# Optimization experiments

Hardware: AMD Instinct MI355X
Metric: run time of the kernel (lower is better)

The kernel has to match this reference:

```python
import math
import jax, jax.numpy as jnp
import numpy as np

TWO_PI = 2.0 * math.pi


def make_coords(H, W):
    """Replicates ConvNet.generate_coordinates -> offsets of shape (9, 2, H, W).
    Pair k gives (dy, dx) for kernel tap k (row-major 3x3); center tap (k=4) is zero."""
    gy, gx = jnp.meshgrid(jnp.arange(H, dtype=jnp.float32),
                          jnp.arange(W, dtype=jnp.float32), indexing='ij')
    cy = H / 2.0 - 0.5
    cx = W / 2.0 - 0.5
    # torch: delta_x along height, delta_y along width; theta = atan2(dy, dx) mod 2pi
    theta = jnp.arctan2(gx - cx, gy - cy) % TWO_PI
    theta = jnp.round(theta * 10000.0) / 10000.0
    # per-tap (angle multiple m of pi/4, additive (ay, ax)); tap 4 (center) stays zero
    taps = [(0, 1.0, 1.0), (1, 1.0, 0.0), (2, 1.0, -1.0), (3, 0.0, 1.0), None,
            (4, 0.0, -1.0), (5, -1.0, 1.0), (6, -1.0, 0.0), (7, -1.0, -1.0)]
    offs = []
    zero = jnp.zeros_like(theta)
    for t in taps:
        if t is None:
            offs.append(jnp.stack([zero, zero]))
        else:
            m, ay, ax = t
            ang = theta + (math.pi / 4.0) * m
            offs.append(jnp.stack([jnp.cos(ang) + ay, jnp.sin(ang) + ax]))
    return jnp.stack(offs)  # (9, 2, H, W)


def deform_conv(x, off, w):
    """torchvision.ops.deform_conv2d, 3x3, stride 1, pad 1, dilation 1, no bias.
    x: (B,C,H,W), off: (9,2,H,W), w: (O,C,3,3) -> (B,O,H,W)."""
    B, C, H, W = x.shape
    ky = jnp.repeat(jnp.arange(3, dtype=jnp.float32), 3)  # (9,)
    kx = jnp.tile(jnp.arange(3, dtype=jnp.float32), 3)
    # sampling positions (H, W, 9)
    py = (jnp.arange(H, dtype=jnp.float32)[:, None, None] - 1.0
          + ky[None, None, :] + jnp.transpose(off[:, 0], (1, 2, 0)))
    px = (jnp.arange(W, dtype=jnp.float32)[None, :, None] - 1.0
          + kx[None, None, :] + jnp.transpose(off[:, 1], (1, 2, 0)))
    y0 = jnp.floor(py)
    x0 = jnp.floor(px)
    wy = py - y0  # bilinear weights
    wx = px - x0

    def gather(yf, xf):
        valid = (yf >= 0) & (yf <= H - 1) & (xf >= 0) & (xf <= W - 1)
        yi = jnp.clip(yf, 0, H - 1).astype(jnp.int32)
        xi = jnp.clip(xf, 0, W - 1).astype(jnp.int32)
        return x[:, :, yi, xi] * valid.astype(x.dtype)  # (B,C,H,W,9)

    sampled = ((1 - wy) * (1 - wx) * gather(y0, x0)
               + (1 - wy) * wx * gather(y0, x0 + 1)
               + wy * (1 - wx) * gather(y0 + 1, x0)
               + wy * wx * gather(y0 + 1, x0 + 1))
    return jnp.einsum('bchwk,ock->bohw', sampled, w.reshape(w.shape[0], C, 9))


def maxpool2(x):
    B, C, H, W = x.shape
    return x.reshape(B, C, H // 2, 2, W // 2, 2).max(axis=(3, 5))


def setup_inputs() -> dict:
    key = jax.random.key(0)
    ks = jax.random.split(key, 20)

    def kaiming(k, shape):
        fan_in = int(np.prod(shape[1:]))
        return jax.random.normal(k, shape, jnp.float32) * np.float32(np.sqrt(2.0 / fan_in))

    inp = {'x': jax.random.normal(ks[0], (8, 3, 128, 128), jnp.float32)}
    conv_shapes = [('w11', (64, 3, 3, 3)), ('w12', (64, 64, 3, 3)),
                   ('w21', (128, 64, 3, 3)), ('w22', (128, 128, 3, 3)),
                   ('w31', (256, 128, 3, 3)), ('w32', (256, 256, 3, 3)), ('w33', (256, 256, 3, 3)),
                   ('w41', (512, 256, 3, 3)), ('w42', (512, 512, 3, 3)), ('w43', (512, 512, 3, 3)),
                   ('w51', (512, 512, 3, 3)), ('w52', (512, 512, 3, 3)), ('w53', (512, 512, 3, 3))]
    for i, (n, s) in enumerate(conv_shapes):
        inp[n] = kaiming(ks[i + 1], s)
    inp['fc1_w'] = kaiming(ks[14], (4096, 512))
    inp['fc1_b'] = jnp.zeros((4096,), jnp.float32)
    inp['fc2_w'] = kaiming(ks[15], (4096, 4096))
    inp['fc2_b'] = jnp.zeros((4096,), jnp.float32)
    inp['fc3_w'] = kaiming(ks[16], (30, 4096))
    inp['fc3_b'] = jnp.zeros((30,), jnp.float32)
    return inp


def reference(x, w11, w12, w21, w22, w31, w32, w33, w41, w42, w43,
              w51, w52, w53, fc1_w, fc1_b, fc2_w, fc2_b, fc3_w, fc3_b):
    c128 = make_coords(128, 128)
    c64 = make_coords(64, 64)
    c32 = make_coords(32, 32)
    c16 = make_coords(16, 16)
    c8 = make_coords(8, 8)
    r = jax.nn.relu
    x = r(deform_conv(x, c128, w11))
    x = r(deform_conv(x, c128, w12))
    x = maxpool2(x)
    x = r(deform_conv(x, c64, w21))
    x = r(deform_conv(x, c64, w22))
    x = maxpool2(x)
    x = r(deform_conv(x, c32, w31))
    x = r(deform_conv(x, c32, w32))
    x = r(deform_conv(x, c32, w33))
    x = maxpool2(x)
    x = r(deform_conv(x, c16, w41))
    x = r(deform_conv(x, c16, w42))
    x = r(deform_conv(x, c16, w43))
    x = maxpool2(x)
    x = r(deform_conv(x, c8, w51))
    x = r(deform_conv(x, c8, w52))
    x = r(deform_conv(x, c8, w53))
    x = maxpool2(x)          # -> (B, 512, 4, 4)
    x = x.mean(axis=(2, 3))  # AvgPool2d((4,4)) on 4x4 -> (B, 512)
    x = r(x @ fc1_w.T + fc1_b)
    x = r(x @ fc2_w.T + fc2_b)
    return x @ fc3_w.T + fc3_b  # (B, 30)
```

## Files before the change

### kernel.cpp

```cpp
#include <hip/hip_runtime.h>
#include <math.h>

#define TWO_PI_F 6.283185307179586f
#define PI_4_F   0.7853981633974483f

typedef __attribute__((ext_vector_type(8))) short short8;
typedef __attribute__((ext_vector_type(4))) float f32x4;
typedef __attribute__((ext_vector_type(2))) float f32x2;
typedef __attribute__((ext_vector_type(4))) unsigned short ushort4v;
typedef __attribute__((ext_vector_type(4))) unsigned int uint4v;
typedef __attribute__((ext_vector_type(2))) unsigned int uint2v;

struct Tap { int i00, i01, i10, i11; float w00, w01, w10, w11; };

static __device__ __forceinline__ unsigned short f2bf(float f) {
    unsigned u = __builtin_bit_cast(unsigned, f);
    u = (u + 0x7fffu + ((u >> 16) & 1u)) >> 16;
    return (unsigned short)u;
}
static __device__ __forceinline__ float bf2f(unsigned short u) {
    return __builtin_bit_cast(float, (unsigned)u << 16);
}
static __device__ __forceinline__ f32x2 up2(unsigned u) {
    f32x2 r;
    r.x = __builtin_bit_cast(float, u << 16);
    r.y = __builtin_bit_cast(float, u & 0xffff0000u);
    return r;
}
static __device__ __forceinline__ unsigned cvt_pk_bf16(float lo, float hi) {
    unsigned r;
    asm("v_cvt_pk_bf16_f32 %0, %1, %2" : "=v"(r) : "v"(lo), "v"(hi));
    return r;
}

__global__ void build_table_kernel(Tap* __restrict__ tab, int* __restrict__ tabA, int S) {
    int idx = blockIdx.x * blockDim.x + threadIdx.x;
    int total = S * S * 9;
    if (idx >= total) return;
    int k = idx % 9;
    int p = idx / 9;
    int y = p / S;
    int x = p - y * S;
    int HW = S * S;

    float c = 0.5f * (float)S - 0.5f;
    float theta = atan2f((float)x - c, (float)y - c);
    theta = fmodf(theta, TWO_PI_F);
    if (theta < 0.0f) theta += TWO_PI_F;
    theta = rintf(theta * 10000.0f) / 10000.0f;

    float offy = 0.0f, offx = 0.0f;
    if (k != 4) {
        int m = (k < 4) ? k : (k - 1);
        const float ayt[8] = { 1.f, 1.f,  1.f, 0.f,  0.f, -1.f, -1.f, -1.f };
        const float axt[8] = { 1.f, 0.f, -1.f, 1.f, -1.f,  1.f,  0.f, -1.f };
        float ang = theta + PI_4_F * (float)m;
        offy = cosf(ang) + ayt[m];
        offx = sinf(ang) + axt[m];
    }
    int ky = k / 3, kx = k - ky * 3;
    float py = (float)y - 1.0f + (float)ky + offy;
    float px = (float)x - 1.0f + (float)kx + offx;
    float fy0 = floorf(py), fx0 = floorf(px);
    float wy = py - fy0, wx = px - fx0;
    float fmaxc = (float)(S - 1);

    Tap t;
    {
        float yy = fy0, xx = fx0;
        bool v = (yy >= 0.f) && (yy <= fmaxc) && (xx >= 0.f) && (xx <= fmaxc);
        int yi = (int)fminf(fmaxf(yy, 0.f), fmaxc);
        int xi = (int)fminf(fmaxf(xx, 0.f), fmaxc);
        t.i00 = yi * S + xi;
        t.w00 = v ? (1.f - wy) * (1.f - wx) : 0.f;
    }
    {
        float yy = fy0, xx = fx0 + 1.0f;
        bool v = (yy >= 0.f) && (yy <= fmaxc) && (xx >= 0.f) && (xx <= fmaxc);
        int yi = (int)fminf(fmaxf(yy, 0.f), fmaxc);
        int xi = (int)fminf(fmaxf(xx, 0.f), fmaxc);
        t.i01 = yi * S + xi;
        t.w01 = v ? (1.f - wy) * wx : 0.f;
    }
    {
        float yy = fy0 + 1.0f, xx = fx0;
        bool v = (yy >= 0.f) && (yy <= fmaxc) && (xx >= 0.f) && (xx <= fmaxc);
        int yi = (int)fminf(fmaxf(yy, 0.f), fmaxc);
        int xi = (int)fminf(fmaxf(xx, 0.f), fmaxc);
        t.i10 = yi * S + xi;
        t.w10 = v ? wy * (1.f - wx) : 0.f;
    }
    {
        float yy = fy0 + 1.0f, xx = fx0 + 1.0f;
        bool v = (yy >= 0.f) && (yy <= fmaxc) && (xx >= 0.f) && (xx <= fmaxc);
        int yi = (int)fminf(fmaxf(yy, 0.f), fmaxc);
        int xi = (int)fminf(fmaxf(xx, 0.f), fmaxc);
        t.i11 = yi * S + xi;
        t.w11 = v ? wy * wx : 0.f;
    }
    tab[idx] = t;

    int rec = (k * HW + p) * 8;
    tabA[rec + 0] = t.i00;
    tabA[rec + 1] = t.i01;
    tabA[rec + 2] = t.i10;
    tabA[rec + 3] = t.i11;
    tabA[rec + 4] = __builtin_bit_cast(int, t.w00);
    tabA[rec + 5] = __builtin_bit_cast(int, t.w01);
    tabA[rec + 6] = __builtin_bit_cast(int, t.w10);
    tabA[rec + 7] = __builtin_bit_cast(int, t.w11);
}

__global__ void pack_w_kernel(const float* __restrict__ w, unsigned short* __restrict__ wP,
                              int O, int C, int total) {
    int idx = blockIdx.x * blockDim.x + threadIdx.x;
    if (idx >= total) return;
    int ksub = idx & 31;
    int kbo  = idx >> 5;
    int o  = kbo % O;
    int kb = kbo / O;
    int K = kb * 32 + ksub;
    int kt = K / C;
    int c  = K - kt * C;
    wP[idx] = f2bf(w[((size_t)o * C + c) * 9 + kt]);
}

__global__ __launch_bounds__(256) void dconv_f32_kernel(
    const float* __restrict__ x, const float* __restrict__ w,
    const Tap* __restrict__ tab, unsigned short* __restrict__ out,
    int C, int O, int HW)
{
    __shared__ float4 sTabRaw[64 * 9 * 2];
    __shared__ float  sS[9][64];
    __shared__ float  sW[9][64];

    const int tid = threadIdx.x;
    const int b  = blockIdx.z;
    const int o0 = blockIdx.y * 64;
    const int p0 = blockIdx.x * 64;
    const int C9 = C * 9;

    const float4* gt = (const float4*)(tab + (size_t)p0 * 9);
    for (int i = tid; i < 64 * 9 * 2; i += 256) sTabRaw[i] = gt[i];
    const Tap* sTab = (const Tap*)sTabRaw;
    __syncthreads();

    float acc[4][4];
#pragma unroll
    for (int i = 0; i < 4; ++i)
#pragma unroll
        for (int j = 0; j < 4; ++j) acc[i][j] = 0.f;

    const int to = tid >> 4;
    const int tn = tid & 15;
    const float* xb = x + (size_t)b * C * HW;

    for (int c = 0; c < C; ++c) {
        const float* xp = xb + (size_t)c * HW;
        for (int i = tid; i < 9 * 64; i += 256) {
            int k = i >> 6;
            int p = i & 63;
            Tap t = sTab[p * 9 + k];
            sS[k][p] = t.w00 * xp[t.i00] + t.w01 * xp[t.i01]
                     + t.w10 * xp[t.i10] + t.w11 * xp[t.i11];
        }
        for (int i = tid; i < 9 * 64; i += 256) {
            int k = i >> 6;
            int o = i & 63;
            sW[k][o] = w[(size_t)(o0 + o) * C9 + c * 9 + k];
        }
        __syncthreads();
#pragma unroll
        for (int k = 0; k < 9; ++k) {
            float4 wv = *(const float4*)&sW[k][to * 4];
            float4 sv = *(const float4*)&sS[k][tn * 4];
            acc[0][0] += wv.x * sv.x; acc[0][1] += wv.x * sv.y; acc[0][2] += wv.x * sv.z; acc[0][3] += wv.x * sv.w;
            acc[1][0] += wv.y * sv.x; acc[1][1] += wv.y * sv.y; acc[1][2] += wv.y * sv.z; acc[1][3] += wv.y * sv.w;
            acc[2][0] += wv.z * sv.x; acc[2][1] += wv.z * sv.y; acc[2][2] += wv.z * sv.z; acc[2][3] += wv.z * sv.w;
            acc[3][0] += wv.w * sv.x; acc[3][1] += wv.w * sv.y; acc[3][2] += wv.w * sv.z; acc[3][3] += wv.w * sv.w;
        }
        __syncthreads();
    }

    const int ob   = (o0 + to * 4) >> 3;
    const int osub = (to & 1) << 2;
#pragma unroll
    for (int j = 0; j < 4; ++j) {
        int p = p0 + tn * 4 + j;
        ushort4v v;
        v.x = f2bf(fmaxf(acc[0][j], 0.f));
        v.y = f2bf(fmaxf(acc[1][j], 0.f));
        v.z = f2bf(fmaxf(acc[2][j], 0.f));
        v.w = f2bf(fmaxf(acc[3][j], 0.f));
        *(ushort4v*)(out + (((size_t)b * (O >> 3) + ob) * HW + p) * 8 + osub) = v;
    }
}

#define SPITCH 296

template<int BM>
__global__ __launch_bounds__(256, 4) void dconv_mfma(
    const unsigned short* __restrict__ x, const unsigned short* __restrict__ wP,
    const int* __restrict__ tabA, unsigned short* __restrict__ out,
    float* __restrict__ part,
    int C, int O, int HW, int Cchunk, int nChunks)
{
    __shared__ unsigned short sS[64 * SPITCH];

    const int tid  = threadIdx.x;
    const int lane = tid & 63;
    const int wv   = tid >> 6;
    const int bz = blockIdx.z;
    const int b     = bz & 7;
    const int chunk = bz >> 3;

    int bx = blockIdx.x;
    const int gx = gridDim.x;
    if ((gx & 7) == 0) { int g8 = gx >> 3; bx = (bx & 7) * g8 + (bx >> 3); }

    const int o0 = blockIdx.y * BM;
    const int p0 = bx * 64;
    const int c0 = chunk * Cchunk;
    const int nGroups = Cchunk >> 5;

    const int o0w = (BM == 128) ? wv * 32 : (wv >> 1) * 32;
    const int p0w = (BM == 128) ? 0       : (wv & 1) * 32;
    constexpr int MF = 2;
    constexpr int NF = (BM == 128) ? 4 : 2;

    f32x4 acc[MF][NF] = {};

    const unsigned short* xb = x + (size_t)b * C * HW;
    const int quad = lane >> 4;
    const int l16  = lane & 15;
    const int* tq = tabA + (((size_t)(p0 + lane)) << 3);
    unsigned short* srow = &sS[lane * SPITCH + (wv << 3)];

    for (int g = 0; g < nGroups; ++g) {
        const int cg = c0 + g * 32;
        const unsigned short* xcb = xb + ((((size_t)(cg >> 3) + wv) * HW) << 3);

#pragma unroll 3
        for (int kt = 0; kt < 9; ++kt) {
            const int* tp = tq + kt * (HW << 3);
            int4 ii = *(const int4*)tp;
            int4 iw = *(const int4*)(tp + 4);
            float w00 = __builtin_bit_cast(float, iw.x);
            float w01 = __builtin_bit_cast(float, iw.y);
            float w10 = __builtin_bit_cast(float, iw.z);
            float w11 = __builtin_bit_cast(float, iw.w);
            uint4v g00 = *(const uint4v*)(xcb + ((size_t)ii.x << 3));
            uint4v g01 = *(const uint4v*)(xcb + ((size_t)ii.y << 3));
            uint4v g10 = *(const uint4v*)(xcb + ((size_t)ii.z << 3));
            uint4v g11 = *(const uint4v*)(xcb + ((size_t)ii.w << 3));
            uint4v pk;
#pragma unroll
            for (int wd = 0; wd < 4; ++wd) {
                f32x2 s = up2(g00[wd]) * w00 + up2(g01[wd]) * w01
                        + up2(g10[wd]) * w10 + up2(g11[wd]) * w11;
                pk[wd] = cvt_pk_bf16(s.x, s.y);
            }
            *(uint4v*)(srow + kt * 32) = pk;
        }
        __syncthreads();

#pragma unroll 3
        for (int kt = 0; kt < 9; ++kt) {
            const int kb = (kt * C + cg) >> 5;
            short8 afr[MF], bfr[NF];
#pragma unroll
            for (int mf = 0; mf < MF; ++mf) {
                int orow = o0 + o0w + mf * 16 + l16;
                afr[mf] = *(const short8*)(wP + (((size_t)kb * O + orow) << 5) + (quad << 3));
            }
#pragma unroll
            for (int nf = 0; nf < NF; ++nf) {
                int prow = p0w + nf * 16 + l16;
                bfr[nf] = *(const short8*)(&sS[prow * SPITCH + kt * 32 + (quad << 3)]);
            }
#pragma unroll
            for (int mf = 0; mf < MF; ++mf)
#pragma unroll
                for (int nf = 0; nf < NF; ++nf)
                    acc[mf][nf] = __builtin_amdgcn_mfma_f32_16x16x32_bf16(afr[mf], bfr[nf], acc[mf][nf], 0, 0, 0);
        }
        __syncthreads();
    }

    const int O8 = O >> 3;
    if (nChunks == 1) {
#pragma unroll
        for (int mf = 0; mf < MF; ++mf)
#pragma unroll
            for (int nf = 0; nf < NF; ++nf) {
                int o = o0 + o0w + mf * 16 + (quad << 2);
                int p = p0 + p0w + nf * 16 + l16;
                size_t base = (((size_t)b * O8 + (o >> 3)) * HW + p) * 8 + (o & 7);
                uint2v pk2;
                pk2.x = cvt_pk_bf16(fmaxf(acc[mf][nf][0], 0.f), fmaxf(acc[mf][nf][1], 0.f));
                pk2.y = cvt_pk_bf16(fmaxf(acc[mf][nf][2], 0.f), fmaxf(acc[mf][nf][3], 0.f));
                *(uint2v*)(out + base) = pk2;
            }
    } else {
        float* pb = part + (size_t)chunk * 8 * O * HW;
#pragma unroll
        for (int mf = 0; mf < MF; ++mf)
#pragma unroll
            for (int nf = 0; nf < NF; ++nf) {
                int o = o0 + o0w + mf * 16 + (quad << 2);
                int p = p0 + p0w + nf * 16 + l16;
                size_t base = (((size_t)b * O8 + (o >> 3)) * HW + p) * 8 + (o & 7);
                *(f32x4*)(pb + base) = acc[mf][nf];
            }
    }
}

__global__ void reduce_relu_kernel(const float* __restrict__ part,
                                   unsigned short* __restrict__ out,
                                   int per4, int nChunks)
{
    int idx = blockIdx.x * blockDim.x + threadIdx.x;
    if (idx >= per4) return;
    const float4* p4 = (const float4*)part;
    float4 s = p4[idx];
    for (int ch = 1; ch < nChunks; ++ch) {
        float4 v = p4[(size_t)ch * per4 + idx];
        s.x += v.x; s.y += v.y; s.z += v.z; s.w += v.w;
    }
    ushort4v r;
    r.x = f2bf(fmaxf(s.x, 0.f)); r.y = f2bf(fmaxf(s.y, 0.f));
    r.z = f2bf(fmaxf(s.z, 0.f)); r.w = f2bf(fmaxf(s.w, 0.f));
    ((ushort4v*)out)[idx] = r;
}

__global__ void reduce_relu_pool_kernel(const float* __restrict__ part,
                                        unsigned short* __restrict__ out,
                                        int S, int per, int nChunks, int total)
{
    int idx = blockIdx.x * blockDim.x + threadIdx.x;
    if (idx >= total) return;
    int Sl = 31 - __clz(S);
    int W2 = S >> 1;
    int c8 = idx & 7;
    int t  = idx >> 3;
    int x2 = t & (W2 - 1); t >>= (Sl - 1);
    int y2 = t & (W2 - 1); t >>= (Sl - 1);
    size_t base = (((size_t)t * S + 2 * y2) * S + 2 * x2) * 8 + c8;
    size_t dX = 8;
    size_t dY = (size_t)S * 8;
    float s0 = 0.f, s1 = 0.f, s2 = 0.f, s3 = 0.f;
    for (int ch = 0; ch < nChunks; ++ch) {
        const float* p = part + (size_t)ch * per + base;
        s0 += p[0]; s1 += p[dX]; s2 += p[dY]; s3 += p[dY + dX];
    }
    out[idx] = f2bf(fmaxf(fmaxf(fmaxf(s0, s1), fmaxf(s2, s3)), 0.f));
}

__global__ void maxpool_kernel(const unsigned short* __restrict__ in,
                               unsigned short* __restrict__ out,
                               int S, int total)
{
    int idx = blockIdx.x * blockDim.x + threadIdx.x;
    if (idx >= total) return;
    int Sl = 31 - __clz(S);
    int W2 = S >> 1;
    int c8 = idx & 7;
    int t  = idx >> 3;
    int x2 = t & (W2 - 1); t >>= (Sl - 1);
    int y2 = t & (W2 - 1); t >>= (Sl - 1);
    size_t base = (((size_t)t * S + 2 * y2) * S + 2 * x2) * 8 + c8;
    size_t dY = (size_t)S * 8;
    const unsigned short* p = in + base;
    float m = fmaxf(fmaxf(bf2f(p[0]), bf2f(p[8])), fmaxf(bf2f(p[dY]), bf2f(p[dY + 8])));
    out[idx] = f2bf(m);
}

__global__ void avgpool_kernel(const unsigned short* __restrict__ in,
                               float* __restrict__ out, int total)
{
    int idx = blockIdx.x * blockDim.x + threadIdx.x;
    if (idx >= total) return;
    int b = idx >> 9;
    int c = idx & 511;
    int cb = c >> 3, c8 = c & 7;
    const unsigned short* p = in + (((size_t)(b * 64 + cb) * 16) << 3) + c8;
    float s = 0.f;
#pragma unroll
    for (int i = 0; i < 16; ++i) s += bf2f(p[i * 8]);
    out[idx] = s * (1.0f / 16.0f);
}

__global__ __launch_bounds__(256) void fc_kernel(
    const float* __restrict__ x, const float* __restrict__ w,
    const float* __restrict__ bias, float* __restrict__ out,
    int K, int O, int relu)
{
    int o = blockIdx.x;
    float acc[8] = {0.f,0.f,0.f,0.f,0.f,0.f,0.f,0.f};
    const float* wr = w + (size_t)o * K;
    for (int k = threadIdx.x; k < K; k += 256) {
        float wv = wr[k];
#pragma unroll
        for (int b = 0; b < 8; ++b) acc[b] += wv * x[(size_t)b * K + k];
    }
    __shared__ float red[8][256];
#pragma unroll
    for (int b = 0; b < 8; ++b) red[b][threadIdx.x] = acc[b];
    __syncthreads();
    for (int s = 128; s > 0; s >>= 1) {
        if (threadIdx.x < s) {
#pragma unroll
            for (int b = 0; b < 8; ++b) red[b][threadIdx.x] += red[b][threadIdx.x + s];
        }
        __syncthreads();
    }
    if (threadIdx.x < 8) {
        float v = red[threadIdx.x][0] + bias[o];
        if (relu) v = fmaxf(v, 0.f);
        out[(size_t)threadIdx.x * O + o] = v;
    }
}

extern "C" void kernel_launch(void* const* d_in, const int* in_sizes, int n_in,
                              void* d_out, int out_size, void* d_ws, size_t ws_size,
                              hipStream_t stream) {
    const float* x    = (const float*)d_in[0];
    const float* wf[13];
    for (int i = 0; i < 13; ++i) wf[i] = (const float*)d_in[1 + i];
    const float* fc1w = (const float*)d_in[14];
    const float* fc1b = (const float*)d_in[15];
    const float* fc2w = (const float*)d_in[16];
    const float* fc2b = (const float*)d_in[17];
    const float* fc3w = (const float*)d_in[18];
    const float* fc3b = (const float*)d_in[19];
    float* out = (float*)d_out;

    char* ws = (char*)d_ws;
    auto alloc = [&](size_t bytes) -> char* {
        char* p = ws;
        ws += (bytes + 255) & ~(size_t)255;
        return p;
    };

    const int sizes[5] = {128, 64, 32, 16, 8};
    Tap* tabs[5];
    int* tabAs[5];
    for (int i = 0; i < 5; ++i) {
        int HW = sizes[i] * sizes[i];
        tabs[i]  = (Tap*)alloc((size_t)HW * 9 * sizeof(Tap));
        tabAs[i] = (int*)alloc((size_t)HW * 9 * 8 * sizeof(int));
    }
    unsigned short* actA = (unsigned short*)alloc((size_t)8 * 64 * 128 * 128 * 2);
    unsigned short* actB = (unsigned short*)alloc((size_t)8 * 64 * 128 * 128 * 2);
    float* partial = (float*)alloc((size_t)2 * 8 * 128 * 4096 * sizeof(float));
    const int Cs[13] = {3, 64, 64, 128, 128, 256, 256, 256, 512, 512, 512, 512, 512};
    const int Os[13] = {64, 64, 128, 128, 256, 256, 256, 512, 512, 512, 512, 512, 512};
    unsigned short* wPk[13];
    wPk[0] = nullptr;
    for (int i = 1; i < 13; ++i)
        wPk[i] = (unsigned short*)alloc((size_t)Os[i] * Cs[i] * 9 * sizeof(unsigned short));
    float* pooled = (float*)alloc((size_t)8 * 512 * sizeof(float));
    float* fcb1 = (float*)alloc((size_t)8 * 4096 * sizeof(float));
    float* fcb2 = (float*)alloc((size_t)8 * 4096 * sizeof(float));

    for (int i = 0; i < 5; ++i) {
        int total = sizes[i] * sizes[i] * 9;
        build_table_kernel<<<(total + 255) / 256, 256, 0, stream>>>(tabs[i], tabAs[i], sizes[i]);
    }
    for (int i = 1; i < 13; ++i) {
        int total = Os[i] * Cs[i] * 9;
        pack_w_kernel<<<(total + 255) / 256, 256, 0, stream>>>(wf[i], wPk[i], Os[i], Cs[i], total);
    }

    auto convM = [&](const unsigned short* in, const unsigned short* wp, int* tabA,
                     unsigned short* o, int C, int O, int S, int nCh, int BM, bool leavePartial) {
        int HW = S * S;
        int Cchunk = C / nCh;
        if (BM == 64) {
            dim3 grid(HW / 64, O / 64, 8 * nCh);
            dconv_mfma<64><<<grid, 256, 0, stream>>>(in, wp, tabA, o, partial, C, O, HW, Cchunk, nCh);
        } else {
            dim3 grid(HW / 64, O / 128, 8 * nCh);
            dconv_mfma<128><<<grid, 256, 0, stream>>>(in, wp, tabA, o, partial, C, O, HW, Cchunk, nCh);
        }
        if (nCh > 1 && !leavePartial) {
            int per4 = 8 * O * HW / 4;
            reduce_relu_kernel<<<(per4 + 255) / 256, 256, 0, stream>>>(partial, o, per4, nCh);
        }
    };
    auto fusedPool = [&](unsigned short* o, int C, int H, int nCh) {
        int per = 8 * C * H * H;
        int total = per / 4;
        reduce_relu_pool_kernel<<<(total + 255) / 256, 256, 0, stream>>>(partial, o, H, per, nCh, total);
    };

    {
        dim3 grid(128 * 128 / 64, 1, 8);
        dconv_f32_kernel<<<grid, 256, 0, stream>>>(x, wf[0], tabs[0], actA, 3, 64, 128 * 128);
    }
    convM(actA, wPk[1],  tabAs[0], actB, 64,  64,  128, 1, 64, false);
    {
        int total = 8 * 64 * 64 * 64;
        maxpool_kernel<<<(total + 255) / 256, 256, 0, stream>>>(actB, actA, 128, total);
    }
    convM(actA, wPk[2],  tabAs[1], actB, 64,  128, 64, 2, 128, false);
    convM(actB, wPk[3],  tabAs[1], nullptr, 128, 128, 64, 2, 128, true);
    fusedPool(actA, 128, 64, 2);
    convM(actA, wPk[4],  tabAs[2], actB, 128, 256, 32, 4, 128, false);
    convM(actB, wPk[5],  tabAs[2], actA, 256, 256, 32, 4, 128, false);
    convM(actA, wPk[6],  tabAs[2], nullptr, 256, 256, 32, 4, 128, true);
    fusedPool(actB, 256, 32, 4);
    convM(actB, wPk[7],  tabAs[3], actA, 256, 512, 16, 8, 128, false);
    convM(actA, wPk[8],  tabAs[3], actB, 512, 512, 16, 8, 128, false);
    convM(actB, wPk[9],  tabAs[3], nullptr, 512, 512, 16, 8, 128, true);
    fusedPool(actA, 512, 16, 8);
    convM(actA, wPk[10], tabAs[4], actB, 512, 512, 8, 16, 64, false);
    convM(actB, wPk[11], tabAs[4], actA, 512, 512, 8, 16, 64, false);
    convM(actA, wPk[12], tabAs[4], nullptr, 512, 512, 8, 16, 64, true);
    fusedPool(actB, 512, 8, 16);

    avgpool_kernel<<<(4096 + 255) / 256, 256, 0, stream>>>(actB, pooled, 8 * 512);

    fc_kernel<<<4096, 256, 0, stream>>>(pooled, fc1w, fc1b, fcb1, 512,  4096, 1);
    fc_kernel<<<4096, 256, 0, stream>>>(fcb1,   fc2w, fc2b, fcb2, 4096, 4096, 1);
    fc_kernel<<<30,   256, 0, stream>>>(fcb2,   fc3w, fc3b, out,  4096, 30,   0);
}
```

Before: 700.0 us.

## Batch table/weight-pack launches and hoist tap indices, skip center-tap interpolation

Merges the five per-scale table-building launches into one 2D-grid launch, and the twelve weight-packing launches into one launch that uses a cumulative-offset lookup. In the MFMA deformable conv kernel, the per-tap gather indices are loaded once into registers before the channel-group loop instead of being reloaded for every group. The center tap (offset zero) becomes a direct copy with no bilinear blend. The aim is to cut launch overhead and redundant table loads, at the cost of higher register pressure from holding nine int4 values.

```diff
diff --git a/kernel.cpp b/kernel.cpp
--- a/kernel.cpp
+++ b/kernel.cpp
@@ -33,10 +33,18 @@
     return r;
 }
 
-__global__ void build_table_kernel(Tap* __restrict__ tab, int* __restrict__ tabA, int S) {
+struct TabPtrs { Tap* tab[5]; int* tabA[5]; };
+
+__global__ void build_table_all(TabPtrs tp) {
+    const int Ss[5] = {128, 64, 32, 16, 8};
+    int si = blockIdx.y;
+    int S = Ss[si];
     int idx = blockIdx.x * blockDim.x + threadIdx.x;
     int total = S * S * 9;
     if (idx >= total) return;
+    Tap* __restrict__ tab  = tp.tab[si];
+    int* __restrict__ tabA = tp.tabA[si];
+
     int k = idx % 9;
     int p = idx / 9;
     int y = p / S;
@@ -111,18 +119,33 @@
     tabA[rec + 7] = __builtin_bit_cast(int, t.w11);
 }
 
-__global__ void pack_w_kernel(const float* __restrict__ w, unsigned short* __restrict__ wP,
-                              int O, int C, int total) {
+struct PackArgs {
+    const float* w[12];
+    unsigned short* wP[12];
+    int O[12];
+    int C[12];
+    int tot[12];
+};
+
+__global__ void pack_w_all(PackArgs pa, int grand) {
     int idx = blockIdx.x * blockDim.x + threadIdx.x;
-    if (idx >= total) return;
-    int ksub = idx & 31;
-    int kbo  = idx >> 5;
+    if (idx >= grand) return;
+    int li = 0, base = 0;
+#pragma unroll
+    for (int i = 0; i < 11; ++i) {
+        if (idx >= pa.tot[i]) { li = i + 1; base = pa.tot[i]; }
+    }
+    int rel = idx - base;
+    int O = pa.O[li];
+    int C = pa.C[li];
+    int ksub = rel & 31;
+    int kbo  = rel >> 5;
     int o  = kbo % O;
     int kb = kbo / O;
     int K = kb * 32 + ksub;
     int kt = K / C;
     int c  = K - kt * C;
-    wP[idx] = f2bf(w[((size_t)o * C + c) * 9 + kt]);
+    pa.wP[li][rel] = f2bf(pa.w[li][((size_t)o * C + c) * 9 + kt]);
 }
 
 __global__ __launch_bounds__(256) void dconv_f32_kernel(
@@ -235,6 +258,12 @@
     const int l16  = lane & 15;
     const int* tq = tabA + (((size_t)(p0 + lane)) << 3);
     unsigned short* srow = &sS[lane * SPITCH + (wv << 3)];
+    const int HW8 = HW << 3;
+
+    int4 iiA[9];
+#pragma unroll
+    for (int kt = 0; kt < 9; ++kt)
+        iiA[kt] = *(const int4*)(tq + kt * HW8);
 
     for (int g = 0; g < nGroups; ++g) {
         const int cg = c0 + g * 32;
@@ -242,25 +271,28 @@
 
 #pragma unroll 3
         for (int kt = 0; kt < 9; ++kt) {
-            const int* tp = tq + kt * (HW << 3);
-            int4 ii = *(const int4*)tp;
-            int4 iw = *(const int4*)(tp + 4);
-            float w00 = __builtin_bit_cast(float, iw.x);
-            float w01 = __builtin_bit_cast(float, iw.y);
-            float w10 = __builtin_bit_cast(float, iw.z);
-            float w11 = __builtin_bit_cast(float, iw.w);
-            uint4v g00 = *(const uint4v*)(xcb + ((size_t)ii.x << 3));
-            uint4v g01 = *(const uint4v*)(xcb + ((size_t)ii.y << 3));
-            uint4v g10 = *(const uint4v*)(xcb + ((size_t)ii.z << 3));
-            uint4v g11 = *(const uint4v*)(xcb + ((size_t)ii.w << 3));
-            uint4v pk;
-#pragma unroll
-            for (int wd = 0; wd < 4; ++wd) {
-                f32x2 s = up2(g00[wd]) * w00 + up2(g01[wd]) * w01
-                        + up2(g10[wd]) * w10 + up2(g11[wd]) * w11;
-                pk[wd] = cvt_pk_bf16(s.x, s.y);
+            int4 ii = iiA[kt];
+            if (kt == 4) {
+                *(uint4v*)(srow + kt * 32) = *(const uint4v*)(xcb + ((size_t)ii.x << 3));
+            } else {
+                int4 iw = *(const int4*)(tq + kt * HW8 + 4);
+                float w00 = __builtin_bit_cast(float, iw.x);
+                float w01 = __builtin_bit_cast(float, iw.y);
+                float w10 = __builtin_bit_cast(float, iw.z);
+                float w11 = __builtin_bit_cast(float, iw.w);
+                uint4v g00 = *(const uint4v*)(xcb + ((size_t)ii.x << 3));
+                uint4v g01 = *(const uint4v*)(xcb + ((size_t)ii.y << 3));
+                uint4v g10 = *(const uint4v*)(xcb + ((size_t)ii.z << 3));
+                uint4v g11 = *(const uint4v*)(xcb + ((size_t)ii.w << 3));
+                uint4v pk;
+#pragma unroll
+                for (int wd = 0; wd < 4; ++wd) {
+                    f32x2 s = up2(g00[wd]) * w00 + up2(g01[wd]) * w01
+                            + up2(g10[wd]) * w10 + up2(g11[wd]) * w11;
+                    pk[wd] = cvt_pk_bf16(s.x, s.y);
+                }
+                *(uint4v*)(srow + kt * 32) = pk;
             }
-            *(uint4v*)(srow + kt * 32) = pk;
         }
         __syncthreads();
 
@@ -463,13 +495,24 @@
     float* fcb1 = (float*)alloc((size_t)8 * 4096 * sizeof(float));
     float* fcb2 = (float*)alloc((size_t)8 * 4096 * sizeof(float));
 
-    for (int i = 0; i < 5; ++i) {
-        int total = sizes[i] * sizes[i] * 9;
-        build_table_kernel<<<(total + 255) / 256, 256, 0, stream>>>(tabs[i], tabAs[i], sizes[i]);
-    }
-    for (int i = 1; i < 13; ++i) {
-        int total = Os[i] * Cs[i] * 9;
-        pack_w_kernel<<<(total + 255) / 256, 256, 0, stream>>>(wf[i], wPk[i], Os[i], Cs[i], total);
+    {
+        TabPtrs tp;
+        for (int i = 0; i < 5; ++i) { tp.tab[i] = tabs[i]; tp.tabA[i] = tabAs[i]; }
+        dim3 grid((128 * 128 * 9 + 255) / 256, 5);
+        build_table_all<<<grid, 256, 0, stream>>>(tp);
+    }
+    {
+        PackArgs pa;
+        int cum = 0;
+        for (int i = 0; i < 12; ++i) {
+            pa.w[i]  = wf[i + 1];
+            pa.wP[i] = wPk[i + 1];
+            pa.O[i]  = Os[i + 1];
+            pa.C[i]  = Cs[i + 1];
+            cum += Os[i + 1] * Cs[i + 1] * 9;
+            pa.tot[i] = cum;
+        }
+        pack_w_all<<<(cum + 255) / 256, 256, 0, stream>>>(pa, cum);
     }
 
     auto convM = [&](const unsigned short* in, const unsigned short* wp, int* tabA,
```

Result: slower. 775.3 us (+10.8%).
